# Performance work log

Measured on AMD Instinct MI355X. Metric: run time of the kernel, lower is better.

The kernel has to match this reference:

```python
import jax, jax.numpy as jnp
import numpy as np
import math

H = 4096; HQ = 32; HK = 8; HV = 8
DQ = H // HQ          # 128
DV = H // HV          # 512 (as defined in the original module)
S = 2048; B = 2


def setup_inputs() -> dict:
    key = jax.random.key(0)
    ks = jax.random.split(key, 9)
    sc = 0.02
    x = jax.random.normal(ks[0], (B, S, H), jnp.float32)
    mask = jnp.triu(jnp.ones((S, S), jnp.bool_), k=1)  # True = masked (causal)
    WQ_w = jax.random.normal(ks[1], (DQ * HQ, H), jnp.float32) * sc
    WQ_b = jax.random.normal(ks[2], (DQ * HQ,), jnp.float32) * sc
    WK_w = jax.random.normal(ks[3], (DQ * HK, H), jnp.float32) * sc
    WK_b = jax.random.normal(ks[4], (DQ * HK,), jnp.float32) * sc
    WV_w = jax.random.normal(ks[5], (DV * HV, H), jnp.float32) * sc
    WV_b = jax.random.normal(ks[6], (DV * HV,), jnp.float32) * sc
    W0_w = jax.random.normal(ks[7], (H, HQ * DV), jnp.float32) * sc
    W0_b = jax.random.normal(ks[8], (H,), jnp.float32) * sc
    return {"x": x, "mask": mask, "WQ_w": WQ_w, "WQ_b": WQ_b, "WK_w": WK_w,
            "WK_b": WK_b, "WV_w": WV_w, "WV_b": WV_b, "W0_w": W0_w, "W0_b": W0_b}


def reference(x, mask, WQ_w, WQ_b, WK_w, WK_b, WV_w, WV_b, W0_w, W0_b):
    b, s, d = x.shape
    g_k = HQ // HK  # query groups per key head
    g_v = HQ // HV
    # Raw row-major reshapes, faithful to the original torch code
    Q = (x @ WQ_w.T + WQ_b).reshape(b, g_k, HK, s, DQ)
    K = (x @ WK_w.T + WK_b).reshape(b, HK, s, DQ)
    V = (x @ WV_w.T + WV_b).reshape(b, HV, s, DV)
    # (B,g,Hk,S,S) via broadcasted GQA matmul, then flatten heads
    attn = jnp.einsum('bghsd,bhtd->bghst', Q, K).reshape(b, HQ, s, s)
    attn = attn / math.sqrt(DQ)
    attn = jnp.where(mask[None, None], -jnp.inf, attn)
    attn = jax.nn.softmax(attn, axis=-1)
    ctx = jnp.einsum('bghst,bhtd->bghsd', attn.reshape(b, g_v, HV, s, s), V)
    out = ctx.reshape(b, s, HQ * DV) @ W0_w.T + W0_b
    return out
```

## Files before the change

kernel.cpp:

```cpp
#include <hip/hip_runtime.h>
#include <stdint.h>

typedef __bf16 bf16;
typedef bf16 bf16x8 __attribute__((ext_vector_type(8)));
typedef float f32x4 __attribute__((ext_vector_type(4)));
typedef int int4v __attribute__((ext_vector_type(4)));
typedef uint32_t u32;

#define DEV static __device__ __forceinline__
#define SBAR() __builtin_amdgcn_s_barrier()

DEV void g2l16(const void* g, void* l) {
  __builtin_amdgcn_global_load_lds((__attribute__((address_space(1))) void*)g,
                                   (__attribute__((address_space(3))) void*)l, 16, 0, 0);
}

DEV u32 pkbf16(float a, float b) {
  union { bf16 h[2]; u32 w; } u;
  u.h[0] = (bf16)a; u.h[1] = (bf16)b;
  return u.w;
}

DEV float fexp2(float x) { return __builtin_amdgcn_exp2f(x); }

__global__ void cvt_bf16(const float* __restrict__ in, bf16* __restrict__ out, int n8) {
  const int i = blockIdx.x * 256 + threadIdx.x;
  if (i >= n8) return;
  const f32x4* p = (const f32x4*)in + (size_t)i * 2;
  const f32x4 a = p[0], b = p[1];
  bf16x8 o;
  o[0]=(bf16)a[0]; o[1]=(bf16)a[1]; o[2]=(bf16)a[2]; o[3]=(bf16)a[3];
  o[4]=(bf16)b[0]; o[5]=(bf16)b[1]; o[6]=(bf16)b[2]; o[7]=(bf16)b[3];
  ((bf16x8*)out)[i] = o;
}

template<int MO, int NO>
DEV void mmaq(f32x4 (&acc)[8][4], const bf16x8 (&af)[4][2], const bf16x8 (&bf)[2][2]) {
#pragma unroll
  for (int m2 = 0; m2 < 4; ++m2)
#pragma unroll
    for (int n2 = 0; n2 < 2; ++n2)
#pragma unroll
      for (int kk = 0; kk < 2; ++kk)
        acc[MO + m2][NO + n2] = __builtin_amdgcn_mfma_f32_16x16x32_bf16(
            af[m2][kk], bf[n2][kk], acc[MO + m2][NO + n2], 0, 0, 0);
}

template<int OUT_BF16>
__global__ __launch_bounds__(512, 2)
void gemm256(const bf16* __restrict__ A, const bf16* __restrict__ Bt,
             void* __restrict__ Cout, const float* __restrict__ bias,
             int M, int N, int K) {
  __shared__ __align__(16) char L[131072];
  const int tid = threadIdx.x, lane = tid & 63, wid = tid >> 6;
  const int wm = wid >> 2, wn = wid & 3;
  const int q = lane & 15, g = lane >> 4;
  const int mt = M >> 8;
  const int nwg = gridDim.x, bid = blockIdx.x;
  const int wg = (bid & 7) * (nwg >> 3) + (bid >> 3);
  const int bm = wg % mt, bn = wg / mt;
  const size_t Kb = (size_t)K * 2;
  const char* Ab = (const char*)A + (size_t)bm * 256 * Kb;
  const char* Bb = (const char*)Bt + (size_t)bn * 256 * Kb;
  const int NT = K >> 6;

  const int csw0 = (g ^ (q & 7)) << 4;
  const int csw1 = ((4 + g) ^ (q & 7)) << 4;
  const int baseA0 = wm * 16384 + q * 128;
  const int baseA1 = 65536 + baseA0;
  const int bBq = 32768 + (wn >> 1) * 16384 + (wn & 1) * 8192 + q * 128;
  const int baseB0 = bBq, baseB1 = 65536 + bBq;

#define RD_A(AF, BASE) do { _Pragma("unroll") \
  for (int m2_ = 0; m2_ < 4; ++m2_) { \
    (AF)[m2_][0] = *(const bf16x8*)(L + (BASE) + m2_ * 2048 + csw0); \
    (AF)[m2_][1] = *(const bf16x8*)(L + (BASE) + m2_ * 2048 + csw1); } } while (0)
#define RD_B(BF, BASE) do { _Pragma("unroll") \
  for (int n2_ = 0; n2_ < 2; ++n2_) { \
    (BF)[n2_][0] = *(const bf16x8*)(L + (BASE) + n2_ * 2048 + csw0); \
    (BF)[n2_][1] = *(const bf16x8*)(L + (BASE) + n2_ * 2048 + csw1); } } while (0)

  auto stage = [&](const char* gb, int ldsHalfBase, int halfRow, int tt) {
#pragma unroll
    for (int r2 = 0; r2 < 2; ++r2) {
      const int rel = r2 * 8192 + wid * 1024;
      const int o = rel + (lane << 4);
      const int row = o >> 7;
      const int kbyte = (o & 127) ^ ((row & 7) << 4);
      g2l16(gb + (size_t)(halfRow * 128 + row) * Kb + (size_t)(tt * 128 + kbyte),
            L + ldsHalfBase + rel);
    }
  };

  f32x4 acc[8][4];
  const f32x4 zero = {0.f, 0.f, 0.f, 0.f};
#pragma unroll
  for (int m = 0; m < 8; ++m)
#pragma unroll
    for (int n = 0; n < 4; ++n) acc[m][n] = zero;
  bf16x8 af[4][2], bflo[2][2], bfhi[2][2];

  stage(Bb, 32768, 0, 0);          stage(Bb, 32768 + 16384, 1, 0);
  stage(Ab, 0, 0, 0);              stage(Ab, 16384, 1, 0);
  stage(Bb, 65536 + 32768, 0, 1);  stage(Bb, 65536 + 32768 + 16384, 1, 1);

  for (int t = 0; t < NT; t += 2) {
    const int tc1 = t + 1;
    const int tc2 = (t + 2 < NT) ? t + 2 : NT - 1;
    const int tc3 = (t + 3 < NT) ? t + 3 : NT - 1;
    asm volatile("s_waitcnt vmcnt(4)" ::: "memory");
    SBAR();
    RD_A(af, baseA0);
    RD_B(bflo, baseB0);
    RD_B(bfhi, baseB0 + 4096);
    stage(Ab, 65536, 0, tc1);
    SBAR();
    __builtin_amdgcn_s_setprio(1);
    mmaq<0, 0>(acc, af, bflo);
    __builtin_amdgcn_s_setprio(0);
    SBAR();
    stage(Ab, 65536 + 16384, 1, tc1);
    SBAR();
    __builtin_amdgcn_s_setprio(1);
    mmaq<0, 2>(acc, af, bfhi);
    __builtin_amdgcn_s_setprio(0);
    SBAR();
    RD_A(af, baseA0 + 8192);
    stage(Bb, 32768, 0, tc2);
    SBAR();
    __builtin_amdgcn_s_setprio(1);
    mmaq<4, 0>(acc, af, bflo);
    __builtin_amdgcn_s_setprio(0);
    SBAR();
    stage(Bb, 32768 + 16384, 1, tc2);
    SBAR();
    __builtin_amdgcn_s_setprio(1);
    mmaq<4, 2>(acc, af, bfhi);
    __builtin_amdgcn_s_setprio(0);
    SBAR();
    asm volatile("s_waitcnt vmcnt(4)" ::: "memory");
    SBAR();
    RD_A(af, baseA1);
    RD_B(bflo, baseB1);
    RD_B(bfhi, baseB1 + 4096);
    stage(Ab, 0, 0, tc2);
    SBAR();
    __builtin_amdgcn_s_setprio(1);
    mmaq<0, 0>(acc, af, bflo);
    __builtin_amdgcn_s_setprio(0);
    SBAR();
    stage(Ab, 16384, 1, tc2);
    SBAR();
    __builtin_amdgcn_s_setprio(1);
    mmaq<0, 2>(acc, af, bfhi);
    __builtin_amdgcn_s_setprio(0);
    SBAR();
    RD_A(af, baseA1 + 8192);
    stage(Bb, 65536 + 32768, 0, tc3);
    SBAR();
    __builtin_amdgcn_s_setprio(1);
    mmaq<4, 0>(acc, af, bflo);
    __builtin_amdgcn_s_setprio(0);
    SBAR();
    stage(Bb, 65536 + 32768 + 16384, 1, tc3);
    SBAR();
    __builtin_amdgcn_s_setprio(1);
    mmaq<4, 2>(acc, af, bfhi);
    __builtin_amdgcn_s_setprio(0);
    SBAR();
  }
  asm volatile("s_waitcnt vmcnt(0)" ::: "memory");

  const int row0 = bm * 256 + wm * 128 + g * 4;
  const int col0 = bn * 256 + wn * 64 + q;
#pragma unroll
  for (int n = 0; n < 4; ++n) {
    const int col = col0 + n * 16;
    const float bv = bias[col];
#pragma unroll
    for (int m = 0; m < 8; ++m) {
#pragma unroll
      for (int r = 0; r < 4; ++r) {
        const int row = row0 + m * 16 + r;
        const float v = acc[m][n][r] + bv;
        if (OUT_BF16) ((bf16*)Cout)[(size_t)row * N + col] = (bf16)v;
        else          ((float*)Cout)[(size_t)row * N + col] = v;
      }
    }
  }
#undef RD_A
#undef RD_B
}

template<int OUT_BF16>
__global__ __launch_bounds__(256, 2)
void gemm_bt(const bf16* __restrict__ A, const bf16* __restrict__ Bt,
             void* __restrict__ Cout, const float* __restrict__ bias,
             int M, int N, int K) {
  __shared__ __align__(16) char As[16384];
  __shared__ __align__(16) char Bs[16384];
  const int tid  = threadIdx.x;
  const int lane = tid & 63;
  const int wid  = tid >> 6;
  const int mt = M >> 7;
  const int nwg = gridDim.x;
  const int bid = blockIdx.x;
  const int wg = (bid & 7) * (nwg >> 3) + (bid >> 3);
  const int bm = wg % mt;
  const int bn = wg / mt;

  const size_t Kb = (size_t)K * 2;
  const char* Ab = (const char*)A + (size_t)bm * 128 * Kb;
  const char* Bb = (const char*)Bt + (size_t)bn * 128 * Kb;

  const int wr = wid >> 1, wc = wid & 1;
  const int q = lane & 15, g = lane >> 4;

  const f32x4 zero = {0.f, 0.f, 0.f, 0.f};
  f32x4 acc[4][4];
#pragma unroll
  for (int m = 0; m < 4; ++m)
#pragma unroll
    for (int n = 0; n < 4; ++n) acc[m][n] = zero;

  for (int k0 = 0; k0 < K; k0 += 64) {
    __syncthreads();
#pragma unroll
    for (int it = 0; it < 4; ++it) {
      const int obase = (it * 4 + wid) << 10;
      const int o = obase + (lane << 4);
      const int row = o >> 7;
      const int kbyte = (o & 127) ^ ((row & 7) << 4);
      g2l16(Ab + (size_t)row * Kb + (size_t)(k0 * 2 + kbyte), As + obase);
      g2l16(Bb + (size_t)row * Kb + (size_t)(k0 * 2 + kbyte), Bs + obase);
    }
    __syncthreads();
#pragma unroll
    for (int kk = 0; kk < 2; ++kk) {
      bf16x8 af[4], bfv[4];
#pragma unroll
      for (int m = 0; m < 4; ++m) {
        const int r = wr * 64 + m * 16 + q;
        const int byte = (r * 128 + kk * 64 + g * 16) ^ ((r & 7) << 4);
        af[m] = *(const bf16x8*)(As + byte);
      }
#pragma unroll
      for (int n = 0; n < 4; ++n) {
        const int r = wc * 64 + n * 16 + q;
        const int byte = (r * 128 + kk * 64 + g * 16) ^ ((r & 7) << 4);
        bfv[n] = *(const bf16x8*)(Bs + byte);
      }
#pragma unroll
      for (int m = 0; m < 4; ++m)
#pragma unroll
        for (int n = 0; n < 4; ++n)
          acc[m][n] = __builtin_amdgcn_mfma_f32_16x16x32_bf16(af[m], bfv[n], acc[m][n], 0, 0, 0);
    }
  }

  const int col0 = bn * 128 + wc * 64 + q;
  const int row0 = bm * 128 + wr * 64 + g * 4;
#pragma unroll
  for (int n = 0; n < 4; ++n) {
    const int col = col0 + n * 16;
    const float bv = bias[col];
#pragma unroll
    for (int m = 0; m < 4; ++m) {
#pragma unroll
      for (int r = 0; r < 4; ++r) {
        const int row = row0 + m * 16 + r;
        const float v = acc[m][n][r] + bv;
        if (OUT_BF16) ((bf16*)Cout)[(size_t)row * N + col] = (bf16)v;
        else          ((float*)Cout)[(size_t)row * N + col] = v;
      }
    }
  }
}

__global__ void transpose_v(const bf16* __restrict__ vlin, bf16* __restrict__ vt) {
  __shared__ __align__(16) bf16 t[64][80];
  const int tid = threadIdx.x;
  const int bh = blockIdx.z;
  const int jt = blockIdx.x, dt = blockIdx.y;
  const bf16* src = vlin + (size_t)bh * 1048576 + (size_t)(jt * 64) * 512 + dt * 64;
  bf16* dst = vt + (size_t)bh * 1048576 + (size_t)(dt * 64) * 2048 + jt * 64;
#pragma unroll
  for (int it = 0; it < 2; ++it) {
    const int c = it * 256 + tid;
    const int r = c >> 3, c8 = (c & 7) * 8;
    *(int4v*)&t[r][c8] = *(const int4v*)(src + (size_t)r * 512 + c8);
  }
  __syncthreads();
#pragma unroll
  for (int it = 0; it < 2; ++it) {
    const int c = it * 256 + tid;
    const int d = c >> 3, j8 = (c & 7) * 8;
    bf16x8 v;
#pragma unroll
    for (int jj = 0; jj < 8; ++jj) v[jj] = t[j8 + jj][d];
    *(bf16x8*)(dst + (size_t)d * 2048 + j8) = v;
  }
}

__global__ __launch_bounds__(512, 2)
void attn(const bf16* __restrict__ Q, const bf16* __restrict__ Kl,
          const bf16* __restrict__ VT, bf16* __restrict__ O) {
  constexpr float SC = 0.08838834764831845f * 1.4426950408889634f;
  __shared__ __align__(16) char L[81920];
  const int tid = threadIdx.x, lane = tid & 63, wid = tid >> 6;
  const int bid = blockIdx.x;
  const int qt = 15 - (bid >> 6);
  const int hq = (bid >> 1) & 31;
  const int b  = bid & 1;
  const int h = hq & 7;
  const char* qb = (const char*)(Q + (((size_t)b * 32 + hq) << 18));
  const char* kb = (const char*)(Kl + (((size_t)b * 8 + h) << 18));
  const char* vb = (const char*)(VT + (((size_t)b * 8 + h) << 20));
  bf16* ob = (bf16*)(O + (((size_t)b * 32 + hq) << 20));

  const int g = lane >> 4, q = lane & 15;
  const int qrow = qt * 128 + wid * 16 + q;
  const float NEGINF = -__builtin_inff();

  auto stageKV = [&](int j0, int bbase) {
    {
      const int obase = wid << 10;
      const int o = obase + (lane << 4);
      const int row = o >> 8;
      const int cb = (o & 255) ^ ((row & 7) << 4);
      g2l16(kb + (size_t)(j0 + row) * 256 + cb, L + bbase + obase);
    }
#pragma unroll
    for (int it = 0; it < 4; ++it) {
      const int obase = (it * 8 + wid) << 10;
      const int o = obase + (lane << 4);
      const int sl = o >> 4;
      const int dpair = sl >> 3;
      const int w2 = (sl & 7) ^ (dpair & 7);
      const int d = dpair * 2 + (w2 >> 2);
      const int jo = w2 & 3;
      g2l16(vb + (size_t)d * 4096 + (size_t)(j0 + jo * 8) * 2,
            L + bbase + 8192 + obase);
    }
  };

  bf16x8 qf[4];
#pragma unroll
  for (int kk = 0; kk < 4; ++kk)
    qf[kk] = *(const bf16x8*)(qb + (size_t)qrow * 256 + kk * 64 + g * 16);

  const f32x4 zero = {0.f, 0.f, 0.f, 0.f};
  f32x4 acc[32];
#pragma unroll
  for (int i = 0; i < 32; ++i) acc[i] = zero;
  float mrun = NEGINF, lrun = 0.f;

  const int ntiles = qt * 4 + 4;
  const int jmax = (ntiles - 1) * 32;
  stageKV(0, 0);
  __syncthreads();
  int bb = 0;

#pragma unroll 1
  for (int jt = 0; jt < ntiles; ++jt) {
    const int j0 = jt * 32;
    const int jn = (j0 < jmax) ? j0 + 32 : jmax;
    stageKV(jn, bb ^ 40960);
    const char* KsB = L + bb;
    const char* VsB = L + bb + 8192;

    f32x4 s0 = zero, s1 = zero;
    __builtin_amdgcn_s_setprio(1);
#pragma unroll
    for (int kk = 0; kk < 4; ++kk) {
      {
        const int r = q;
        const int byte = (r * 256 + kk * 64 + g * 16) ^ ((r & 7) << 4);
        const bf16x8 kf = *(const bf16x8*)(KsB + byte);
        s0 = __builtin_amdgcn_mfma_f32_16x16x32_bf16(kf, qf[kk], s0, 0, 0, 0);
      }
      {
        const int r = 16 + q;
        const int byte = (r * 256 + kk * 64 + g * 16) ^ ((r & 7) << 4);
        const bf16x8 kf = *(const bf16x8*)(KsB + byte);
        s1 = __builtin_amdgcn_mfma_f32_16x16x32_bf16(kf, qf[kk], s1, 0, 0, 0);
      }
    }
    __builtin_amdgcn_s_setprio(0);

    float sv[8];
#pragma unroll
    for (int r = 0; r < 4; ++r) {
      float v0 = s0[r] * SC;
      float v1 = s1[r] * SC;
      if (j0 + g * 4 + r > qrow)      v0 = NEGINF;
      if (j0 + 16 + g * 4 + r > qrow) v1 = NEGINF;
      sv[r] = v0; sv[4 + r] = v1;
    }
    float pmax = fmaxf(fmaxf(fmaxf(sv[0], sv[1]), fmaxf(sv[2], sv[3])),
                       fmaxf(fmaxf(sv[4], sv[5]), fmaxf(sv[6], sv[7])));
    pmax = fmaxf(pmax, __shfl_xor(pmax, 16));
    pmax = fmaxf(pmax, __shfl_xor(pmax, 32));

    if (!__all(pmax <= mrun + 11.5f)) {
      const float mnew = fmaxf(mrun, pmax);
      const float cf = fexp2(mrun - mnew);
      float cfr[4];
#pragma unroll
      for (int r = 0; r < 4; ++r) cfr[r] = __shfl(cf, g * 4 + r);
#pragma unroll
      for (int i = 0; i < 32; ++i) {
        acc[i][0] *= cfr[0]; acc[i][1] *= cfr[1];
        acc[i][2] *= cfr[2]; acc[i][3] *= cfr[3];
      }
      lrun *= cf;
      mrun = mnew;
    }

    u32 u0[2], u1[2];
    {
      const float p0 = fexp2(sv[0] - mrun), p1 = fexp2(sv[1] - mrun);
      const float p2 = fexp2(sv[2] - mrun), p3 = fexp2(sv[3] - mrun);
      const float p4 = fexp2(sv[4] - mrun), p5 = fexp2(sv[5] - mrun);
      const float p6 = fexp2(sv[6] - mrun), p7 = fexp2(sv[7] - mrun);
      lrun += ((p0 + p1) + (p2 + p3)) + ((p4 + p5) + (p6 + p7));
      u0[0] = pkbf16(p0, p1); u0[1] = pkbf16(p2, p3);
      u1[0] = pkbf16(p4, p5); u1[1] = pkbf16(p6, p7);
    }

    u32 aw[4];
#pragma unroll
    for (int i = 0; i < 4; ++i) {
      const int src = ((2 * g + (i >> 1)) & 3) * 16 + q;
      const u32 v0 = (u32)__shfl((int)u0[i & 1], src);
      const u32 v1 = (u32)__shfl((int)u1[i & 1], src);
      aw[i] = (g < 2) ? v0 : v1;
    }
    union { u32 w[4]; bf16x8 v; } pu;
    pu.w[0] = aw[0]; pu.w[1] = aw[1]; pu.w[2] = aw[2]; pu.w[3] = aw[3];
    const bf16x8 pa = pu.v;

    __builtin_amdgcn_s_setprio(1);
#pragma unroll
    for (int nd = 0; nd < 32; ++nd) {
      const int d = nd * 16 + q;
      const int w2 = ((d & 1) * 4 + g) ^ ((d >> 1) & 7);
      const int byte = (d >> 1) * 128 + w2 * 16;
      const bf16x8 vf = *(const bf16x8*)(VsB + byte);
      acc[nd] = __builtin_amdgcn_mfma_f32_16x16x32_bf16(pa, vf, acc[nd], 0, 0, 0);
    }
    __builtin_amdgcn_s_setprio(0);
    __syncthreads();
    bb ^= 40960;
  }

  float lt = lrun + __shfl_xor(lrun, 16);
  lt += __shfl_xor(lt, 32);
  const float linv = 1.f / lt;
  float lr[4];
#pragma unroll
  for (int r = 0; r < 4; ++r) lr[r] = __shfl(linv, g * 4 + r);
#pragma unroll
  for (int nd = 0; nd < 32; ++nd) {
#pragma unroll
    for (int r = 0; r < 4; ++r) {
      const int qq = qt * 128 + wid * 16 + g * 4 + r;
      ob[(size_t)qq * 512 + nd * 16 + q] = (bf16)(acc[nd][r] * lr[r]);
    }
  }
}

extern "C" void kernel_launch(void* const* d_in, const int* in_sizes, int n_in,
                              void* d_out, int out_size, void* d_ws, size_t ws_size,
                              hipStream_t stream) {
  (void)in_sizes; (void)n_in; (void)out_size; (void)ws_size;
  const float* x   = (const float*)d_in[0];
  const float* WQw = (const float*)d_in[2];
  const float* WQb = (const float*)d_in[3];
  const float* WKw = (const float*)d_in[4];
  const float* WKb = (const float*)d_in[5];
  const float* WVw = (const float*)d_in[6];
  const float* WVb = (const float*)d_in[7];
  const float* W0w = (const float*)d_in[8];
  const float* W0b = (const float*)d_in[9];
  float* out = (float*)d_out;

  bf16* ws = (bf16*)d_ws;
  size_t off = 0;
  auto alloc = [&](size_t n) { bf16* p = ws + off; off += n; return p; };
  bf16* xb   = alloc(16777216);
  bf16* wqb  = alloc(16777216);
  bf16* wkb  = alloc(4194304);
  bf16* wvb  = alloc(16777216);
  bf16* w0b  = alloc(67108864);
  bf16* qlin = alloc(16777216);
  bf16* klin = alloc(4194304);
  bf16* vlin = alloc(16777216);
  bf16* vt   = alloc(16777216);
  bf16* ctx  = alloc(67108864);

  cvt_bf16<<<8192,  256, 0, stream>>>(x,   xb,  2097152);
  cvt_bf16<<<8192,  256, 0, stream>>>(WQw, wqb, 2097152);
  cvt_bf16<<<2048,  256, 0, stream>>>(WKw, wkb, 524288);
  cvt_bf16<<<8192,  256, 0, stream>>>(WVw, wvb, 2097152);
  cvt_bf16<<<32768, 256, 0, stream>>>(W0w, w0b, 8388608);

  gemm256<1><<<256, 512, 0, stream>>>(xb, wqb, qlin, WQb, 4096, 4096, 4096);
  gemm_bt<1><<<256, 256, 0, stream>>>(xb, wkb, klin, WKb, 4096, 1024, 4096);
  gemm256<1><<<256, 512, 0, stream>>>(xb, wvb, vlin, WVb, 4096, 4096, 4096);

  transpose_v<<<dim3(32, 8, 16), 256, 0, stream>>>(vlin, vt);

  attn<<<1024, 512, 0, stream>>>(qlin, klin, vt, ctx);

  gemm256<0><<<256, 512, 0, stream>>>(ctx, w0b, out, W0b, 4096, 4096, 16384);
}
```

Before: 1.157 ms.

## Cut barriers in GEMM main loop by batching stages between MFMA blocks

Restructures the GEMM main loop so that each pair of global-to-LDS stage calls is issued together, followed by two MFMA quarter-blocks under one priority raise. Most of the s_barrier calls between stage and MMA phases are removed, and sched_barrier fences keep the compiler from reordering across phases. The A-tile prefetch for the second half is issued earlier, before the waitcnt, which is relaxed to vmcnt(8). The goal is lower barrier and synchronization overhead and more memory/compute overlap. The risk is that the looser waitcnt and the barrier removal could race on LDS buffers if the counts are wrong.

Measured after the change: 1.150 ms. Within noise of the previous version (-0.7%).

```diff
diff --git a/kernel.cpp b/kernel.cpp
--- a/kernel.cpp
+++ b/kernel.cpp
@@ -9,6 +9,7 @@
 
 #define DEV static __device__ __forceinline__
 #define SBAR() __builtin_amdgcn_s_barrier()
+#define SCHED0() __builtin_amdgcn_sched_barrier(0)
 
 DEV void g2l16(const void* g, void* l) {
   __builtin_amdgcn_global_load_lds((__attribute__((address_space(1))) void*)g,
@@ -113,61 +114,40 @@
     RD_A(af, baseA0);
     RD_B(bflo, baseB0);
     RD_B(bfhi, baseB0 + 4096);
-    stage(Ab, 65536, 0, tc1);
-    SBAR();
+    stage(Ab, 65536, 0, tc1);  stage(Ab, 65536 + 16384, 1, tc1);
     __builtin_amdgcn_s_setprio(1);
     mmaq<0, 0>(acc, af, bflo);
-    __builtin_amdgcn_s_setprio(0);
-    SBAR();
-    stage(Ab, 65536 + 16384, 1, tc1);
-    SBAR();
-    __builtin_amdgcn_s_setprio(1);
     mmaq<0, 2>(acc, af, bfhi);
     __builtin_amdgcn_s_setprio(0);
+    SCHED0();
     SBAR();
     RD_A(af, baseA0 + 8192);
-    stage(Bb, 32768, 0, tc2);
+    stage(Bb, 32768, 0, tc2);  stage(Bb, 32768 + 16384, 1, tc2);
+    __builtin_amdgcn_s_setprio(1);
+    mmaq<4, 0>(acc, af, bflo);
+    mmaq<4, 2>(acc, af, bfhi);
+    __builtin_amdgcn_s_setprio(0);
+    SCHED0();
     SBAR();
-    __builtin_amdgcn_s_setprio(1);
-    mmaq<4, 0>(acc, af, bflo);
-    __builtin_amdgcn_s_setprio(0);
-    SBAR();
-    stage(Bb, 32768 + 16384, 1, tc2);
-    SBAR();
-    __builtin_amdgcn_s_setprio(1);
-    mmaq<4, 2>(acc, af, bfhi);
-    __builtin_amdgcn_s_setprio(0);
-    SBAR();
-    asm volatile("s_waitcnt vmcnt(4)" ::: "memory");
+    stage(Ab, 0, 0, tc2);  stage(Ab, 16384, 1, tc2);
+    asm volatile("s_waitcnt vmcnt(8)" ::: "memory");
     SBAR();
     RD_A(af, baseA1);
     RD_B(bflo, baseB1);
     RD_B(bfhi, baseB1 + 4096);
-    stage(Ab, 0, 0, tc2);
-    SBAR();
     __builtin_amdgcn_s_setprio(1);
     mmaq<0, 0>(acc, af, bflo);
-    __builtin_amdgcn_s_setprio(0);
-    SBAR();
-    stage(Ab, 16384, 1, tc2);
-    SBAR();
-    __builtin_amdgcn_s_setprio(1);
     mmaq<0, 2>(acc, af, bfhi);
     __builtin_amdgcn_s_setprio(0);
+    SCHED0();
     SBAR();
     RD_A(af, baseA1 + 8192);
-    stage(Bb, 65536 + 32768, 0, tc3);
-    SBAR();
+    stage(Bb, 65536 + 32768, 0, tc3);  stage(Bb, 65536 + 32768 + 16384, 1, tc3);
     __builtin_amdgcn_s_setprio(1);
     mmaq<4, 0>(acc, af, bflo);
-    __builtin_amdgcn_s_setprio(0);
-    SBAR();
-    stage(Bb, 65536 + 32768 + 16384, 1, tc3);
-    SBAR();
-    __builtin_amdgcn_s_setprio(1);
     mmaq<4, 2>(acc, af, bfhi);
     __builtin_amdgcn_s_setprio(0);
-    SBAR();
+    SCHED0();
   }
   asm volatile("s_waitcnt vmcnt(0)" ::: "memory");
 
```
